# Performance work log

Measured on AMD Instinct MI355X. Metric: run time of the kernel, lower is better.

The kernel has to match this reference:

```python
import jax, jax.numpy as jnp
import numpy as np

D = 1024      # d_model
H = 8         # heads
DH = D // H
L = 12        # layers
E = 4         # experts
F = 2048      # dim_feedforward
NCLS = 10
SPARSITY = 0.5
EPS = 1e-5
B, S = 4, 512


def _xavier(key, shape):
    fan_in, fan_out = shape[-1], shape[-2] if len(shape) > 1 else shape[-1]
    scale = jnp.sqrt(2.0 / (fan_in + fan_out))
    return jax.random.normal(key, shape, jnp.float32) * scale


def setup_inputs() -> dict:
    key = jax.random.key(0)
    ks = jax.random.split(key, 16)
    return {
        "x": jax.random.normal(ks[0], (B, S, D), jnp.float32),
        "pos": jax.random.normal(ks[1], (1, 512, D), jnp.float32) * 0.02,
        # stacked per-layer transformer params
        "Wqkv": _xavier(ks[2], (L, 3 * D, D)), "bqkv": jnp.zeros((L, 3 * D), jnp.float32),
        "Wo": _xavier(ks[3], (L, D, D)),       "bo": jnp.zeros((L, D), jnp.float32),
        "ln1_s": jnp.ones((L, D), jnp.float32), "ln1_b": jnp.zeros((L, D), jnp.float32),
        "W1": _xavier(ks[4], (L, F, D)), "b1": jnp.zeros((L, F), jnp.float32),
        "W2": _xavier(ks[5], (L, D, F)), "b2": jnp.zeros((L, D), jnp.float32),
        "ln2_s": jnp.ones((L, D), jnp.float32), "ln2_b": jnp.zeros((L, D), jnp.float32),
        # shared gate / experts / classifier
        "Wg": _xavier(ks[6], (E, D)), "bg": jnp.zeros((E,), jnp.float32),
        "We": _xavier(ks[7], (E, D, D)), "be": jnp.zeros((E, D), jnp.float32),
        "Wf": _xavier(ks[8], (NCLS, D)), "bf": jnp.zeros((NCLS,), jnp.float32),
    }


def _layernorm(x, s, b):
    m = jnp.mean(x, axis=-1, keepdims=True)
    v = jnp.mean(jnp.square(x - m), axis=-1, keepdims=True)
    return (x - m) * jax.lax.rsqrt(v + EPS) * s + b


def _forward(x, pos, Wqkv, bqkv, Wo, bo, ln1_s, ln1_b, W1, b1, W2, b2,
             ln2_s, ln2_b, Wg, bg, We, be, Wf, bf):
    Bx, Sx, _ = x.shape
    x = x + pos[:, :Sx, :]
    for l in range(L):
        # --- self-attention (post-norm TransformerEncoderLayer, eval/no-dropout) ---
        qkv = x @ Wqkv[l].T + bqkv[l]                      # [B,S,3D]
        q, k, v = jnp.split(qkv, 3, axis=-1)
        q = q.reshape(Bx, Sx, H, DH).transpose(0, 2, 1, 3)  # bhsd
        k = k.reshape(Bx, Sx, H, DH).transpose(0, 2, 1, 3)
        v = v.reshape(Bx, Sx, H, DH).transpose(0, 2, 1, 3)
        attn = jax.nn.softmax(jnp.einsum('bhqd,bhkd->bhqk', q, k) / jnp.sqrt(jnp.float32(DH)), axis=-1)
        o = jnp.einsum('bhqk,bhkd->bhqd', attn, v).transpose(0, 2, 1, 3).reshape(Bx, Sx, D)
        o = o @ Wo[l].T + bo[l]
        x = _layernorm(x + o, ln1_s[l], ln1_b[l])
        # --- ffn (exact gelu) ---
        h = jax.nn.gelu(x @ W1[l].T + b1[l], approximate=False) @ W2[l].T + b2[l]
        x = _layernorm(x + h, ln2_s[l], ln2_b[l])
        # --- top-2 gated MoE (shared gate/experts across layers) ---
        gs = jax.nn.softmax(x @ Wg.T + bg, axis=-1)         # [B,S,E]
        vals, idx = jax.lax.top_k(gs, 2)                    # [B,S,2]
        all_out = jnp.einsum('bsd,eod->bseo', x, We) + be   # [B,S,E,D]
        sel = jnp.take_along_axis(all_out, idx[..., None], axis=2)  # [B,S,2,D]
        expert_out = jnp.sum(sel * vals[..., None], axis=2)
        x = x * (1.0 - SPARSITY) + expert_out * SPARSITY
    return x[:, -1, :] @ Wf.T + bf                          # [B,10]


def reference(x, pos, Wqkv, bqkv, Wo, bo, ln1_s, ln1_b, W1, b1, W2, b2,
              ln2_s, ln2_b, Wg, bg, We, be, Wf, bf):
    return _forward(x, pos, Wqkv, bqkv, Wo, bo, ln1_s, ln1_b, W1, b1, W2, b2,
                    ln2_s, ln2_b, Wg, bg, We, be, Wf, bf)
```

## Files before the change

### kernel.cpp

```cpp
#include <hip/hip_runtime.h>
#include <math.h>

#define D     1024
#define NH    8
#define DHD   128
#define NL    12
#define NE    4
#define FF    2048
#define NCLS  10
#define BB    4
#define SS    512
#define TT    (BB*SS)
#define EPSV  1e-5f
#define SPARS 0.5f

typedef __attribute__((ext_vector_type(8))) short bf16x8;
typedef __attribute__((ext_vector_type(4))) float f32x4;
typedef unsigned short ushortT;

__device__ __forceinline__ ushortT f2bf(float f) {
    unsigned u = __float_as_uint(f);
    u += 0x7FFF + ((u >> 16) & 1);
    return (ushortT)(u >> 16);
}
__device__ __forceinline__ float bf2f(ushortT h) {
    return __uint_as_float(((unsigned)h) << 16);
}

__global__ __launch_bounds__(256)
void wconv(const float* __restrict__ in, ushortT* __restrict__ out, long n)
{
    const long stride = (long)gridDim.x * 256 * 8;
    for (long i = ((long)blockIdx.x * 256 + threadIdx.x) * 8; i < n; i += stride) {
        float f[8];
        *reinterpret_cast<float4*>(f)   = *reinterpret_cast<const float4*>(in + i);
        *reinterpret_cast<float4*>(f+4) = *reinterpret_cast<const float4*>(in + i + 4);
        bf16x8 u;
        #pragma unroll
        for (int e = 0; e < 8; ++e) ((ushortT*)&u)[e] = f2bf(f[e]);
        *reinterpret_cast<bf16x8*>(out + i) = u;
    }
}

#define LDP 40

template<int MODE, int SK, int ACT, int BN, int EPI>
__global__ __launch_bounds__(256)
void gemm_mfma(const ushortT* __restrict__ A, const ushortT* __restrict__ Bw,
               const float* __restrict__ bias, void* __restrict__ Cv,
               int M, int N, int Ktot, int Klen, long eBw, long eBias, long eC,
               float* __restrict__ qp, ushortT* __restrict__ kp, ushortT* __restrict__ vp)
{
    const int z = blockIdx.z;
    int koff = 0;
    float* Cf = nullptr; ushortT* Ch = nullptr;
    if constexpr (SK > 1) {
        koff = z * Klen;
        Cf = (float*)Cv + (size_t)z * M * N;
    } else {
        Bw   += (size_t)z * eBw;
        bias += (size_t)z * eBias;
        if constexpr (MODE == 0) Ch = (ushortT*)Cv + (size_t)z * eC;
        else                     Cf = (float*)Cv   + (size_t)z * eC;
    }

    constexpr int MR = (BN == 128) ? 4 : 2;
    __shared__ ushortT Asl[128 * LDP];
    __shared__ ushortT Bsl[BN * LDP];

    const int tid  = threadIdx.x;
    const int wave = tid >> 6, lane = tid & 63;
    const int wm = (BN == 128) ? (wave >> 1) * 64 : wave * 32;
    const int wn = (BN == 128) ? (wave & 1) * 64 : 0;
    const int fr = lane & 15;
    const int fq = lane >> 4;

    const int m0 = blockIdx.y * 128;
    const int n0 = blockIdx.x * BN;

    const int arow = tid >> 1;
    const int akc  = (tid & 1) * 16;
    const ushortT* Ag = A + (size_t)(m0 + arow) * Ktot + koff + akc;
    const int brow = (BN == 128) ? (tid >> 1) : (tid >> 2);
    const int bkc  = (BN == 128) ? (tid & 1) * 16 : (tid & 3) * 8;
    const ushortT* Bg = Bw + (size_t)(n0 + brow) * Ktot + koff + bkc;

    f32x4 acc[MR][4] = {};
    bf16x8 av8[2], bv8[2];

    av8[0] = *reinterpret_cast<const bf16x8*>(Ag);
    av8[1] = *reinterpret_cast<const bf16x8*>(Ag + 8);
    bv8[0] = *reinterpret_cast<const bf16x8*>(Bg);
    if constexpr (BN == 128)
        bv8[1] = *reinterpret_cast<const bf16x8*>(Bg + 8);

    for (int k0 = 0; k0 < Klen; k0 += 32) {
        __syncthreads();
        *reinterpret_cast<bf16x8*>(&Asl[arow*LDP + akc])     = av8[0];
        *reinterpret_cast<bf16x8*>(&Asl[arow*LDP + akc + 8]) = av8[1];
        *reinterpret_cast<bf16x8*>(&Bsl[brow*LDP + bkc])     = bv8[0];
        if constexpr (BN == 128)
            *reinterpret_cast<bf16x8*>(&Bsl[brow*LDP + bkc + 8]) = bv8[1];
        __syncthreads();

        const int kn = k0 + 32;
        if (kn < Klen) {
            av8[0] = *reinterpret_cast<const bf16x8*>(Ag + kn);
            av8[1] = *reinterpret_cast<const bf16x8*>(Ag + kn + 8);
            bv8[0] = *reinterpret_cast<const bf16x8*>(Bg + kn);
            if constexpr (BN == 128)
                bv8[1] = *reinterpret_cast<const bf16x8*>(Bg + kn + 8);
        }

        bf16x8 af[MR], bfr[4];
        #pragma unroll
        for (int i = 0; i < MR; ++i)
            af[i]  = *reinterpret_cast<const bf16x8*>(&Asl[(wm + i*16 + fr)*LDP + fq*8]);
        #pragma unroll
        for (int j = 0; j < 4; ++j)
            bfr[j] = *reinterpret_cast<const bf16x8*>(&Bsl[(wn + j*16 + fr)*LDP + fq*8]);
        #pragma unroll
        for (int i = 0; i < MR; ++i)
            #pragma unroll
            for (int j = 0; j < 4; ++j)
                acc[i][j] = __builtin_amdgcn_mfma_f32_16x16x32_bf16(af[i], bfr[j], acc[i][j], 0, 0, 0);
    }

    #pragma unroll
    for (int j = 0; j < 4; ++j) {
        const int n = n0 + wn + j*16 + fr;
        float bb = 0.f;
        if constexpr (SK == 1) bb = bias[n];
        #pragma unroll
        for (int i = 0; i < MR; ++i) {
            const int mb = m0 + wm + i*16 + fq*4;
            if constexpr (EPI == 1) {
                #pragma unroll
                for (int r = 0; r < 4; ++r) {
                    const float u = acc[i][j][r] + bb;
                    const int t = mb + r;
                    if (n0 < D) {
                        qp[(size_t)t*D + n] = u;
                    } else if (n0 < 2*D) {
                        const int n2 = n - D;
                        const int hh = n2 >> 7, dd = n2 & 127;
                        const int bb_ = t >> 9, ss_ = t & 511;
                        kp[(((size_t)bb_*NH + hh)*SS + ss_)*DHD + dd] = f2bf(u);
                    } else {
                        vp[(size_t)t*D + (n - 2*D)] = f2bf(u);
                    }
                }
            } else if constexpr (SK > 1) {
                #pragma unroll
                for (int r = 0; r < 4; ++r)
                    Cf[(size_t)(mb + r) * N + n] = acc[i][j][r];
            } else if constexpr (MODE == 0) {
                #pragma unroll
                for (int r = 0; r < 4; ++r) {
                    float u = acc[i][j][r] + bb;
                    if constexpr (ACT == 1) u = 0.5f*u*(1.0f + erff(u*0.70710678118654752f));
                    Ch[(size_t)(mb + r) * N + n] = f2bf(u);
                }
            } else {
                #pragma unroll
                for (int r = 0; r < 4; ++r) {
                    float u = acc[i][j][r] + bb;
                    if constexpr (ACT == 1) u = 0.5f*u*(1.0f + erff(u*0.70710678118654752f));
                    Cf[(size_t)(mb + r) * N + n] = u;
                }
            }
        }
    }
}

__global__ __launch_bounds__(256)
void v_tr(const ushortT* __restrict__ Vb, ushortT* __restrict__ Vt)
{
    __shared__ ushortT T[64*136];
    const int tid = threadIdx.x;
    const int st = blockIdx.x, bh = blockIdx.y;
    const int b = bh >> 3, h = bh & 7;
    const ushortT* base = Vb + (size_t)(b*SS + st*64)*D + h*DHD;

    #pragma unroll
    for (int p = 0; p < 4; ++p) {
        const int row = (tid >> 4) + 16*p;
        const int colb = (tid & 15) * 8;
        bf16x8 u = *reinterpret_cast<const bf16x8*>(base + (size_t)row*D + colb);
        *reinterpret_cast<bf16x8*>(&T[row*136 + colb]) = u;
    }
    __syncthreads();
    #pragma unroll
    for (int p = 0; p < 4; ++p) {
        const int d  = (tid >> 3) + 32*p;
        const int sb = (tid & 7) * 8;
        bf16x8 u;
        #pragma unroll
        for (int e = 0; e < 8; ++e) ((ushortT*)&u)[e] = T[(sb + e)*136 + d];
        *reinterpret_cast<bf16x8*>(&Vt[((size_t)bh*DHD + d)*SS + st*64 + sb]) = u;
    }
}

#define KLP 136
#define VLP 72
#define PLP 72

__global__ __launch_bounds__(256)
void attn_mfma(const float* __restrict__ Qb, const ushortT* __restrict__ Kb,
               const ushortT* __restrict__ Vt, ushortT* __restrict__ o16)
{
    __shared__ ushortT Kl[64*KLP];
    __shared__ ushortT Vl[128*VLP];
    __shared__ ushortT Pl[4*16*PLP];

    const int tid = threadIdx.x;
    const int w = tid >> 6, lane = tid & 63;
    const int g = lane >> 4, c = lane & 15;
    const int bh = blockIdx.y;
    const int b = bh >> 3, h = bh & 7;
    const int q0 = blockIdx.x*64 + w*16;
    ushortT* Pw = Pl + w*16*PLP;

    bf16x8 qhi[4], qlo[4];
    const float scale = 0.08838834764831845f;
    {
        const float* Qrow = Qb + (size_t)(b*SS + q0 + c)*D + h*DHD;
        #pragma unroll
        for (int db = 0; db < 4; ++db) {
            float f[8];
            *reinterpret_cast<float4*>(f)   = *reinterpret_cast<const float4*>(Qrow + db*32 + g*8);
            *reinterpret_cast<float4*>(f+4) = *reinterpret_cast<const float4*>(Qrow + db*32 + g*8 + 4);
            #pragma unroll
            for (int e = 0; e < 8; ++e) {
                const float fs = f[e]*scale;
                const ushortT hi = f2bf(fs);
                ((ushortT*)&qhi[db])[e] = hi;
                ((ushortT*)&qlo[db])[e] = f2bf(fs - bf2f(hi));
            }
        }
    }

    const ushortT* Kg = Kb + (size_t)bh*SS*DHD;
    const ushortT* Vg = Vt + (size_t)bh*DHD*SS;

    float m_r[4], l_r[4];
    #pragma unroll
    for (int r = 0; r < 4; ++r) { m_r[r] = -1e30f; l_r[r] = 0.f; }
    f32x4 oacc[8] = {};

    for (int kt = 0; kt < SS/64; ++kt) {
        __syncthreads();
        #pragma unroll
        for (int p = 0; p < 4; ++p) {
            const int row = (tid >> 4) + 16*p;
            const int colb = (tid & 15)*8;
            bf16x8 u = *reinterpret_cast<const bf16x8*>(&Kg[(size_t)(kt*64 + row)*DHD + colb]);
            *reinterpret_cast<bf16x8*>(&Kl[row*KLP + colb]) = u;
        }
        #pragma unroll
        for (int p = 0; p < 4; ++p) {
            const int dr = (tid >> 3) + 32*p;
            const int sb = (tid & 7)*8;
            bf16x8 u = *reinterpret_cast<const bf16x8*>(&Vg[(size_t)dr*SS + kt*64 + sb]);
            *reinterpret_cast<bf16x8*>(&Vl[dr*VLP + sb]) = u;
        }
        __syncthreads();

        f32x4 s[4] = {};
        #pragma unroll
        for (int db = 0; db < 4; ++db) {
            bf16x8 kf[4];
            #pragma unroll
            for (int kb = 0; kb < 4; ++kb)
                kf[kb] = *reinterpret_cast<const bf16x8*>(&Kl[(kb*16 + c)*KLP + db*32 + g*8]);
            #pragma unroll
            for (int kb = 0; kb < 4; ++kb) {
                s[kb] = __builtin_amdgcn_mfma_f32_16x16x32_bf16(qhi[db], kf[kb], s[kb], 0, 0, 0);
                s[kb] = __builtin_amdgcn_mfma_f32_16x16x32_bf16(qlo[db], kf[kb], s[kb], 0, 0, 0);
            }
        }

        float tmax[4];
        #pragma unroll
        for (int r = 0; r < 4; ++r)
            tmax[r] = fmaxf(fmaxf(s[0][r], s[1][r]), fmaxf(s[2][r], s[3][r]));
        #pragma unroll
        for (int off = 1; off < 16; off <<= 1)
            #pragma unroll
            for (int r = 0; r < 4; ++r)
                tmax[r] = fmaxf(tmax[r], __shfl_xor(tmax[r], off));
        float mn[4], corr[4];
        #pragma unroll
        for (int r = 0; r < 4; ++r) {
            mn[r] = fmaxf(m_r[r], tmax[r]);
            corr[r] = __expf(m_r[r] - mn[r]);
            m_r[r] = mn[r];
        }
        float tsum[4] = {0.f, 0.f, 0.f, 0.f};
        #pragma unroll
        for (int kb = 0; kb < 4; ++kb)
            #pragma unroll
            for (int r = 0; r < 4; ++r) {
                const float p = __expf(s[kb][r] - mn[r]);
                s[kb][r] = p;
                tsum[r] += p;
            }
        #pragma unroll
        for (int off = 1; off < 16; off <<= 1)
            #pragma unroll
            for (int r = 0; r < 4; ++r)
                tsum[r] += __shfl_xor(tsum[r], off);
        #pragma unroll
        for (int r = 0; r < 4; ++r) l_r[r] = l_r[r]*corr[r] + tsum[r];
        #pragma unroll
        for (int df = 0; df < 8; ++df)
            #pragma unroll
            for (int r = 0; r < 4; ++r)
                oacc[df][r] *= corr[r];

        #pragma unroll
        for (int kb = 0; kb < 4; ++kb)
            #pragma unroll
            for (int r = 0; r < 4; ++r)
                Pw[(g*4 + r)*PLP + kb*16 + c] = f2bf(s[kb][r]);

        #pragma unroll
        for (int kk = 0; kk < 2; ++kk) {
            bf16x8 pa = *reinterpret_cast<const bf16x8*>(&Pw[c*PLP + kk*32 + g*8]);
            #pragma unroll
            for (int df = 0; df < 8; ++df) {
                bf16x8 vb = *reinterpret_cast<const bf16x8*>(&Vl[(df*16 + c)*VLP + kk*32 + g*8]);
                oacc[df] = __builtin_amdgcn_mfma_f32_16x16x32_bf16(pa, vb, oacc[df], 0, 0, 0);
            }
        }
    }

    #pragma unroll
    for (int r = 0; r < 4; ++r) {
        const float inv = 1.0f / l_r[r];
        ushortT* orow = o16 + (size_t)(b*SS + q0 + g*4 + r)*D + h*DHD + c;
        #pragma unroll
        for (int df = 0; df < 8; ++df)
            orow[df*16] = f2bf(oacc[df][r] * inv);
    }
}

template<int SK, int GATE>
__global__ __launch_bounds__(256)
void add_ln_r(const float* __restrict__ xin, const float* __restrict__ P,
              const float* __restrict__ dbias,
              const float* __restrict__ gs, const float* __restrict__ gb,
              float* __restrict__ x32, ushortT* __restrict__ x16,
              const float* __restrict__ Wg, const float* __restrict__ bg,
              float* __restrict__ gv, int* __restrict__ gi)
{
    const int row = blockIdx.x, tid = threadIdx.x;
    const size_t off = (size_t)row*D + tid*4;
    float4 a = *reinterpret_cast<const float4*>(xin + off);
    float d0, d1, d2, d3;
    {
        float4 bvd = *reinterpret_cast<const float4*>(dbias + tid*4);
        d0 = bvd.x; d1 = bvd.y; d2 = bvd.z; d3 = bvd.w;
    }
    #pragma unroll
    for (int s = 0; s < SK; ++s) {
        float4 pv = *reinterpret_cast<const float4*>(P + (size_t)s*TT*D + off);
        d0 += pv.x; d1 += pv.y; d2 += pv.z; d3 += pv.w;
    }
    float v0=a.x+d0, v1=a.y+d1, v2=a.z+d2, v3=a.w+d3;
    __shared__ float red[2][4];
    float s = v0+v1+v2+v3;
    #pragma unroll
    for (int o = 32; o; o >>= 1) s += __shfl_xor(s, o, 64);
    if ((tid & 63) == 0) red[0][tid>>6] = s;
    __syncthreads();
    const float mean = (red[0][0]+red[0][1]+red[0][2]+red[0][3]) * (1.0f/D);
    v0-=mean; v1-=mean; v2-=mean; v3-=mean;
    float qv = v0*v0+v1*v1+v2*v2+v3*v3;
    #pragma unroll
    for (int o = 32; o; o >>= 1) qv += __shfl_xor(qv, o, 64);
    if ((tid & 63) == 0) red[1][tid>>6] = qv;
    __syncthreads();
    const float var = (red[1][0]+red[1][1]+red[1][2]+red[1][3]) * (1.0f/D);
    const float rstd = rsqrtf(var + EPSV);
    float4 sv = *reinterpret_cast<const float4*>(gs + tid*4);
    float4 bv = *reinterpret_cast<const float4*>(gb + tid*4);
    float ov[4];
    ov[0] = v0*rstd*sv.x + bv.x;
    ov[1] = v1*rstd*sv.y + bv.y;
    ov[2] = v2*rstd*sv.z + bv.z;
    ov[3] = v3*rstd*sv.w + bv.w;
    float4 o4; o4.x=ov[0]; o4.y=ov[1]; o4.z=ov[2]; o4.w=ov[3];
    *reinterpret_cast<float4*>(x32 + off) = o4;
    ushort4 h4; h4.x=f2bf(ov[0]); h4.y=f2bf(ov[1]); h4.z=f2bf(ov[2]); h4.w=f2bf(ov[3]);
    *reinterpret_cast<ushort4*>(x16 + off) = h4;

    if constexpr (GATE) {
        float p[4] = {0.f, 0.f, 0.f, 0.f};
        #pragma unroll
        for (int e = 0; e < 4; ++e) {
            const float* wr = Wg + (size_t)e*D + tid*4;
            p[e] = ov[0]*wr[0] + ov[1]*wr[1] + ov[2]*wr[2] + ov[3]*wr[3];
        }
        #pragma unroll
        for (int o = 32; o; o >>= 1) {
            p[0] += __shfl_xor(p[0], o, 64); p[1] += __shfl_xor(p[1], o, 64);
            p[2] += __shfl_xor(p[2], o, 64); p[3] += __shfl_xor(p[3], o, 64);
        }
        __shared__ float gred[4][4];
        if ((tid & 63) == 0) {
            const int w = tid>>6;
            gred[w][0]=p[0]; gred[w][1]=p[1]; gred[w][2]=p[2]; gred[w][3]=p[3];
        }
        __syncthreads();
        if (tid == 0) {
            float g[4];
            #pragma unroll
            for (int e = 0; e < 4; ++e) g[e] = gred[0][e]+gred[1][e]+gred[2][e]+gred[3][e] + bg[e];
            const float mx = fmaxf(fmaxf(g[0],g[1]), fmaxf(g[2],g[3]));
            float ssum = 0.f;
            #pragma unroll
            for (int e = 0; e < 4; ++e) { g[e] = __expf(g[e]-mx); ssum += g[e]; }
            const float inv = 1.0f/ssum;
            #pragma unroll
            for (int e = 0; e < 4; ++e) g[e] *= inv;
            int i0 = 0;
            for (int e = 1; e < 4; ++e) if (g[e] > g[i0]) i0 = e;
            int i1 = (i0 == 0) ? 1 : 0;
            for (int e = 0; e < 4; ++e) if (e != i0 && g[e] > g[i1]) i1 = e;
            gv[row*2]   = g[i0]; gv[row*2+1] = g[i1];
            gi[row*2]   = i0;    gi[row*2+1] = i1;
        }
    }
}

__global__ __launch_bounds__(256)
void moe_combine(float* __restrict__ x, ushortT* __restrict__ x16,
                 const float* __restrict__ eo,
                 const float* __restrict__ gv, const int* __restrict__ gi)
{
    const size_t i = (size_t)blockIdx.x*256 + threadIdx.x;
    const int t = (int)(i >> 10);
    const float w0 = gv[t*2]*SPARS, w1 = gv[t*2+1]*SPARS;
    const size_t TD = (size_t)TT*D;
    const float e0 = eo[(size_t)gi[t*2]*TD + i];
    const float e1 = eo[(size_t)gi[t*2+1]*TD + i];
    const float r = x[i]*(1.0f-SPARS) + w0*e0 + w1*e1;
    x[i] = r;
    x16[i] = f2bf(r);
}

__global__ __launch_bounds__(256)
void addpos(const float* __restrict__ xin, const float* __restrict__ pos,
            float* __restrict__ xo, ushortT* __restrict__ x16)
{
    const size_t i = (size_t)blockIdx.x*256 + threadIdx.x;
    const float r = xin[i] + pos[i & ((size_t)SS*D - 1)];
    xo[i] = r;
    x16[i] = f2bf(r);
}

__global__ __launch_bounds__(64)
void final_kernel(const float* __restrict__ x, const float* __restrict__ Wf,
                  const float* __restrict__ bf, float* __restrict__ out)
{
    const int b = blockIdx.x / NCLS, n = blockIdx.x % NCLS;
    const float* xr = x + ((size_t)b*SS + SS-1)*D;
    const int tid = threadIdx.x;
    float s = 0.f;
    for (int d = tid; d < D; d += 64) s += xr[d]*Wf[(size_t)n*D + d];
    #pragma unroll
    for (int o = 32; o; o >>= 1) s += __shfl_xor(s, o, 64);
    if (tid == 0) out[b*NCLS + n] = s + bf[n];
}

extern "C" void kernel_launch(void* const* d_in, const int* in_sizes, int n_in,
                              void* d_out, int out_size, void* d_ws, size_t ws_size,
                              hipStream_t stream)
{
    const float* x_in = (const float*)d_in[0];
    const float* pos  = (const float*)d_in[1];
    const float* Wqkv = (const float*)d_in[2];
    const float* bqkv = (const float*)d_in[3];
    const float* Wo   = (const float*)d_in[4];
    const float* bo   = (const float*)d_in[5];
    const float* ln1s = (const float*)d_in[6];
    const float* ln1b = (const float*)d_in[7];
    const float* W1   = (const float*)d_in[8];
    const float* b1   = (const float*)d_in[9];
    const float* W2   = (const float*)d_in[10];
    const float* b2   = (const float*)d_in[11];
    const float* ln2s = (const float*)d_in[12];
    const float* ln2b = (const float*)d_in[13];
    const float* Wg   = (const float*)d_in[14];
    const float* bg   = (const float*)d_in[15];
    const float* We   = (const float*)d_in[16];
    const float* be   = (const float*)d_in[17];
    const float* Wf   = (const float*)d_in[18];
    const float* bf   = (const float*)d_in[19];
    float* out = (float*)d_out;

    const long nWqkv = (long)NL*3*D*D;
    const long nWo   = (long)NL*D*D;
    const long nW1   = (long)NL*FF*D;
    const long nW2   = (long)NL*D*FF;
    const long nWe   = (long)NE*D*D;

    float* ws     = (float*)d_ws;
    float*   xbuf  = ws;
    ushortT* xb16  = (ushortT*)(xbuf + (size_t)TT*D);
    ushortT* ob16  = xb16 + (size_t)TT*D;
    float*   scratch = (float*)(ob16 + (size_t)TT*D);
    ushortT* hb16 = (ushortT*)(scratch + (size_t)TT*D*4);
    float*   gv    = (float*)(hb16 + (size_t)TT*FF);
    int*     gi    = (int*)(gv + (size_t)TT*2);
    ushortT* wq16  = (ushortT*)(gi + (size_t)TT*2);
    ushortT* wo16  = wq16 + nWqkv;
    ushortT* w116  = wo16 + nWo;
    ushortT* w216  = w116 + nW1;
    ushortT* we16  = w216 + nW2;
    float*   Qbuf = scratch;
    ushortT* Kb   = (ushortT*)(Qbuf + (size_t)TT*D);
    ushortT* Vb   = Kb + (size_t)TT*D;
    ushortT* Vt   = Vb + (size_t)TT*D;
    float*   parts  = scratch;
    float*   ebuf   = scratch;

    const dim3 blk(256);
    wconv<<<dim3(2048), blk, 0, stream>>>(Wqkv, wq16, nWqkv);
    wconv<<<dim3(1024), blk, 0, stream>>>(Wo,   wo16, nWo);
    wconv<<<dim3(2048), blk, 0, stream>>>(W1,   w116, nW1);
    wconv<<<dim3(2048), blk, 0, stream>>>(W2,   w216, nW2);
    wconv<<<dim3(512),  blk, 0, stream>>>(We,   we16, nWe);

    addpos<<<dim3(TT*D/256), blk, 0, stream>>>(x_in, pos, xbuf, xb16);

    for (int l = 0; l < NL; ++l) {
        gemm_mfma<1,1,0,64,1><<<dim3(3*D/64, TT/128, 1), blk, 0, stream>>>(
            xb16, wq16 + (size_t)l*3*D*D, bqkv + (size_t)l*3*D, nullptr,
            TT, 3*D, D, D, 0, 0, 0, Qbuf, Kb, Vb);
        v_tr<<<dim3(SS/64, BB*NH), blk, 0, stream>>>(Vb, Vt);
        attn_mfma<<<dim3(SS/64, BB*NH), blk, 0, stream>>>(Qbuf, Kb, Vt, ob16);
        gemm_mfma<1,4,0,128,0><<<dim3(D/128, TT/128, 4), blk, 0, stream>>>(
            ob16, wo16 + (size_t)l*D*D, bo, parts, TT, D, D, D/4, 0, 0, 0,
            nullptr, nullptr, nullptr);
        add_ln_r<4,0><<<dim3(TT), blk, 0, stream>>>(
            xbuf, parts, bo + (size_t)l*D, ln1s + (size_t)l*D, ln1b + (size_t)l*D,
            xbuf, xb16, nullptr, nullptr, nullptr, nullptr);
        gemm_mfma<0,1,1,64,0><<<dim3(FF/64, TT/128, 1), blk, 0, stream>>>(
            xb16, w116 + (size_t)l*FF*D, b1 + (size_t)l*FF, hb16, TT, FF, D, D, 0, 0, 0,
            nullptr, nullptr, nullptr);
        gemm_mfma<1,4,0,128,0><<<dim3(D/128, TT/128, 4), blk, 0, stream>>>(
            hb16, w216 + (size_t)l*D*FF, b2, parts, TT, D, FF, FF/4, 0, 0, 0,
            nullptr, nullptr, nullptr);
        add_ln_r<4,1><<<dim3(TT), blk, 0, stream>>>(
            xbuf, parts, b2 + (size_t)l*D, ln2s + (size_t)l*D, ln2b + (size_t)l*D,
            xbuf, xb16, Wg, bg, gv, gi);
        gemm_mfma<1,1,0,64,0><<<dim3(D/64, TT/128, NE), blk, 0, stream>>>(
            xb16, we16, be, ebuf, TT, D, D, D, (long)D*D, (long)D, (long)TT*D,
            nullptr, nullptr, nullptr);
        moe_combine<<<dim3(TT*D/256), blk, 0, stream>>>(xbuf, xb16, ebuf, gv, gi);
    }
    final_kernel<<<dim3(BB*NCLS), dim3(64), 0, stream>>>(xbuf, Wf, bf, out);
}
```

Measured before the change: 2.422 ms.

## Load GEMM tiles directly into LDS with global_load_lds, dropping register staging

Replaces the register-staged global-to-LDS copy in the MFMA GEMM with direct global_load_lds 16-byte transfers issued per wave. The padded LDS row stride is removed so rows are packed at 32 elements. The intent is to cut VGPR use and the separate LDS store instructions. In exchange it loses the register prefetch of the next K tile, so global load latency is no longer overlapped with MFMA work. The unpadded layout may also raise LDS bank conflicts on fragment reads.

```diff
diff --git a/kernel.cpp b/kernel.cpp
--- a/kernel.cpp
+++ b/kernel.cpp
@@ -27,6 +27,11 @@
     return __uint_as_float(((unsigned)h) << 16);
 }
 
+#define GLOAD16(gp, lp) \
+    __builtin_amdgcn_global_load_lds( \
+        (__attribute__((address_space(1))) const void*)(gp), \
+        (__attribute__((address_space(3))) void*)(lp), 16, 0, 0)
+
 __global__ __launch_bounds__(256)
 void wconv(const float* __restrict__ in, ushortT* __restrict__ out, long n)
 {
@@ -42,7 +47,6 @@
     }
 }
 
-#define LDP 40
 
 template<int MODE, int SK, int ACT, int BN, int EPI>
 __global__ __launch_bounds__(256)
@@ -65,8 +69,8 @@
     }
 
     constexpr int MR = (BN == 128) ? 4 : 2;
-    __shared__ ushortT Asl[128 * LDP];
-    __shared__ ushortT Bsl[BN * LDP];
+    __shared__ __align__(16) ushortT Asl[128 * 32];
+    __shared__ __align__(16) ushortT Bsl[BN * 32];
 
     const int tid  = threadIdx.x;
     const int wave = tid >> 6, lane = tid & 63;
@@ -78,47 +82,42 @@
     const int m0 = blockIdx.y * 128;
     const int n0 = blockIdx.x * BN;
 
-    const int arow = tid >> 1;
-    const int akc  = (tid & 1) * 16;
-    const ushortT* Ag = A + (size_t)(m0 + arow) * Ktot + koff + akc;
-    const int brow = (BN == 128) ? (tid >> 1) : (tid >> 2);
-    const int bkc  = (BN == 128) ? (tid & 1) * 16 : (tid & 3) * 8;
-    const ushortT* Bg = Bw + (size_t)(n0 + brow) * Ktot + koff + bkc;
+    const int lrow = lane >> 2;
+    const int lkc  = (lane & 3) * 8;
+    const ushortT* AgA = A + (size_t)(m0 + wave*32 + lrow) * Ktot + koff + lkc;
+    const ushortT* AgB = AgA + (size_t)16 * Ktot;
+    ushortT* AlA = &Asl[(wave*32)      * 32];
+    ushortT* AlB = &Asl[(wave*32 + 16) * 32];
+    const ushortT* BgA;
+    const ushortT* BgB = nullptr;
+    ushortT* BlA; ushortT* BlB = nullptr;
+    if constexpr (BN == 128) {
+        BgA = Bw + (size_t)(n0 + wave*32 + lrow) * Ktot + koff + lkc;
+        BgB = BgA + (size_t)16 * Ktot;
+        BlA = &Bsl[(wave*32)      * 32];
+        BlB = &Bsl[(wave*32 + 16) * 32];
+    } else {
+        BgA = Bw + (size_t)(n0 + wave*16 + lrow) * Ktot + koff + lkc;
+        BlA = &Bsl[(wave*16) * 32];
+    }
 
     f32x4 acc[MR][4] = {};
-    bf16x8 av8[2], bv8[2];
-
-    av8[0] = *reinterpret_cast<const bf16x8*>(Ag);
-    av8[1] = *reinterpret_cast<const bf16x8*>(Ag + 8);
-    bv8[0] = *reinterpret_cast<const bf16x8*>(Bg);
-    if constexpr (BN == 128)
-        bv8[1] = *reinterpret_cast<const bf16x8*>(Bg + 8);
 
     for (int k0 = 0; k0 < Klen; k0 += 32) {
         __syncthreads();
-        *reinterpret_cast<bf16x8*>(&Asl[arow*LDP + akc])     = av8[0];
-        *reinterpret_cast<bf16x8*>(&Asl[arow*LDP + akc + 8]) = av8[1];
-        *reinterpret_cast<bf16x8*>(&Bsl[brow*LDP + bkc])     = bv8[0];
-        if constexpr (BN == 128)
-            *reinterpret_cast<bf16x8*>(&Bsl[brow*LDP + bkc + 8]) = bv8[1];
+        GLOAD16(AgA + k0, AlA);
+        GLOAD16(AgB + k0, AlB);
+        GLOAD16(BgA + k0, BlA);
+        if constexpr (BN == 128) GLOAD16(BgB + k0, BlB);
         __syncthreads();
 
-        const int kn = k0 + 32;
-        if (kn < Klen) {
-            av8[0] = *reinterpret_cast<const bf16x8*>(Ag + kn);
-            av8[1] = *reinterpret_cast<const bf16x8*>(Ag + kn + 8);
-            bv8[0] = *reinterpret_cast<const bf16x8*>(Bg + kn);
-            if constexpr (BN == 128)
-                bv8[1] = *reinterpret_cast<const bf16x8*>(Bg + kn + 8);
-        }
-
         bf16x8 af[MR], bfr[4];
         #pragma unroll
         for (int i = 0; i < MR; ++i)
-            af[i]  = *reinterpret_cast<const bf16x8*>(&Asl[(wm + i*16 + fr)*LDP + fq*8]);
+            af[i]  = *reinterpret_cast<const bf16x8*>(&Asl[(wm + i*16 + fr)*32 + fq*8]);
         #pragma unroll
         for (int j = 0; j < 4; ++j)
-            bfr[j] = *reinterpret_cast<const bf16x8*>(&Bsl[(wn + j*16 + fr)*LDP + fq*8]);
+            bfr[j] = *reinterpret_cast<const bf16x8*>(&Bsl[(wn + j*16 + fr)*32 + fq*8]);
         #pragma unroll
         for (int i = 0; i < MR; ++i)
             #pragma unroll
```

Result: slower. 2.502 ms (+3.3%).
